# Optimization experiments

Measured on AMD Instinct MI355X. Metric: run time of the kernel, lower is better.

Reference implementation:

```python
import jax, jax.numpy as jnp
import numpy as np

N, D, E, L, H, F1, G, A = 4096, 256, 131072, 3, 4, 128, 16, 32

def setup_inputs() -> dict:
    key = jax.random.key(0)
    ks = jax.random.split(key, 12)
    s = lambda k, shape, fan: jax.random.normal(k, shape, jnp.float32) / np.sqrt(fan)
    return {
        "x": jax.random.normal(ks[0], (N, D), jnp.float32),
        "edge_attr": jax.random.uniform(ks[1], (E,), jnp.float32),
        "conv_Wself": s(ks[2], (L, D, D), D),
        "conv_Wnbr": s(ks[3], (L, D, D), D),
        "conv_b": jnp.zeros((L, D), jnp.float32),
        "bn_gamma": jnp.ones((L - 1, D), jnp.float32),
        "bn_beta": jnp.zeros((L - 1, D), jnp.float32),
        "bn_mean": jnp.zeros((L - 1, D), jnp.float32),
        "bn_var": jnp.ones((L - 1, D), jnp.float32),
        "Wqkv": s(ks[4], (3, D, D), D),
        "bqkv": jnp.zeros((3, D), jnp.float32),
        "Wo": s(ks[5], (D, D), D),
        "bo": jnp.zeros((D,), jnp.float32),
        "fc1_W": s(ks[6], (D, F1), D),
        "fc1_b": jnp.zeros((F1,), jnp.float32),
        "AW1": s(ks[7], (G, F1, A), F1),
        "Ab1": jnp.zeros((G, A), jnp.float32),
        "AW2": s(ks[8], (G, A, 1), A),
        "Ab2": jnp.zeros((G, 1), jnp.float32),
        "edge_index": jax.random.randint(ks[9], (2, E), 0, N, jnp.int32),
        "node_groups": jax.random.randint(ks[10], (N,), 0, G, jnp.int32),
    }


def reference(x, edge_attr, conv_Wself, conv_Wnbr, conv_b, bn_gamma, bn_beta,
              bn_mean, bn_var, Wqkv, bqkv, Wo, bo, fc1_W, fc1_b,
              AW1, Ab1, AW2, Ab2, edge_index, node_groups):
    src, dst = edge_index[0], edge_index[1]
    # message-passing conv stack (edge_attr only used by the last, non-attention layer)
    for i in range(L):
        msg = x[src]
        if i == L - 1:
            msg = msg * edge_attr[:, None]
        agg = jax.ops.segment_sum(msg, dst, num_segments=N)
        x = x @ conv_Wself[i] + agg @ conv_Wnbr[i] + conv_b[i]
        if i < L - 1:
            x = bn_gamma[i] * (x - bn_mean[i]) * jax.lax.rsqrt(bn_var[i] + 1e-5) + bn_beta[i]
            x = jax.nn.elu(x)
    # hierarchy self-attention over all N nodes (batch of 1), residual add
    dh = D // H
    q = (x @ Wqkv[0] + bqkv[0]).reshape(N, H, dh)
    k = (x @ Wqkv[1] + bqkv[1]).reshape(N, H, dh)
    v = (x @ Wqkv[2] + bqkv[2]).reshape(N, H, dh)
    scores = jnp.einsum('nhd,mhd->hnm', q, k) / np.sqrt(dh).astype(np.float32)
    attn = jax.nn.softmax(scores, axis=-1)
    o = jnp.einsum('hnm,mhd->nhd', attn, v).reshape(N, D) @ Wo + bo
    x = x + o
    feats = jax.nn.elu(x @ fc1_W + fc1_b)  # [N, F1]; dropout is eval no-op
    # MoE-style per-node group adapter routing: gather tiny MLP weights per node
    h = jax.nn.relu(jnp.einsum('nd,nda->na', feats, AW1[node_groups]) + Ab1[node_groups])
    out = jnp.einsum('na,nao->no', h, AW2[node_groups]) + Ab2[node_groups]  # [N, 1]
    return out
```

## Files before the change

kernel.cpp:

```cpp
#include <hip/hip_runtime.h>
#include <math.h>

#define NN   4096
#define DIM  256
#define NE   131072
#define NH   4
#define DH   64
#define F1D  128
#define NG   16
#define AD   32

typedef unsigned short u16;
typedef unsigned int   u32;
typedef _Float16 f16;
typedef __attribute__((ext_vector_type(8))) _Float16 half8;
typedef __attribute__((ext_vector_type(4))) float f32x4;

enum { EPI_BIAS = 0, EPI_BNELU = 1 };
enum { MEPI_WO = 0, MEPI_FC1 = 1 };

#define MFMA16(a, b, c) __builtin_amdgcn_mfma_f32_16x16x32_f16(a, b, c, 0, 0, 0)

__device__ inline u16 f2h(float x) { union { f16 f; u16 u; } c; c.f = (f16)x; return c.u; }
__device__ inline void split16(float x, u16& h, u16& l) {
    union { f16 f; u16 u; } ch, cl;
    ch.f = (f16)x;
    cl.f = (f16)(x - (float)ch.f);
    h = ch.u; l = cl.u;
}

__global__ void csr_count(const int* __restrict__ dst, int* __restrict__ cnt) {
    int e = blockIdx.x * 256 + threadIdx.x;
    atomicAdd(&cnt[dst[e]], 1);
}

__global__ __launch_bounds__(1024) void csr_scan(
    int* __restrict__ cnt, int* __restrict__ off)
{
    __shared__ int wsum[16];
    const int t = threadIdx.x;
    const int lane = t & 63;
    int4 v = *(const int4*)&cnt[t * 4];
    const int s = v.x + v.y + v.z + v.w;
    int acc = s;
    #pragma unroll
    for (int o = 1; o < 64; o <<= 1) {
        int u = __shfl_up(acc, o);
        if (lane >= o) acc += u;
    }
    if (lane == 63) wsum[t >> 6] = acc;
    __syncthreads();
    if (t < 16) {
        int w0 = wsum[t];
        int a2 = w0;
        #pragma unroll
        for (int o = 1; o < 16; o <<= 1) {
            int u = __shfl_up(a2, o);
            if (t >= o) a2 += u;
        }
        wsum[t] = a2 - w0;
    }
    __syncthreads();
    const int base = wsum[t >> 6] + (acc - s);
    off[t * 4 + 0] = base;
    off[t * 4 + 1] = base + v.x;
    off[t * 4 + 2] = base + v.x + v.y;
    off[t * 4 + 3] = base + v.x + v.y + v.z;
    *(int4*)&cnt[t * 4] = make_int4(0, 0, 0, 0);
    if (t == 1023) off[NN] = base + s;
}

__global__ void csr_fill(const int* __restrict__ dst, const int* __restrict__ src,
                         const float* __restrict__ eattr, const int* __restrict__ off,
                         int* __restrict__ cur, int* __restrict__ esrc,
                         float* __restrict__ ewt) {
    int e = blockIdx.x * 256 + threadIdx.x;
    int d = dst[e];
    int pos = off[d] + atomicAdd(&cur[d], 1);
    esrc[pos] = src[e];
    ewt[pos]  = eattr[e];
}

__global__ __launch_bounds__(256) void prep_kernel(
    const float* __restrict__ x,
    const float* __restrict__ Ws, const float* __restrict__ Wn,
    const float* __restrict__ Wqkv, const float* __restrict__ Wo,
    const float* __restrict__ fc1W,
    u16* __restrict__ xh, u16* __restrict__ xl,
    u16* __restrict__ wch, u16* __restrict__ wcl,
    u16* __restrict__ w4h, u16* __restrict__ w4l,
    u16* __restrict__ f1h, u16* __restrict__ f1l,
    int* __restrict__ cur)
{
    const int b = blockIdx.x;
    const int t = threadIdx.x;
    if (b < 1024) {
        const int gid = b * 256 + t;
        const float4 v = *(const float4*)&x[(size_t)gid * 4];
        u16 h[4], l[4];
        split16(v.x, h[0], l[0]); split16(v.y, h[1], l[1]);
        split16(v.z, h[2], l[2]); split16(v.w, h[3], l[3]);
        *(uint2*)&xh[(size_t)gid * 4] =
            make_uint2((u32)h[0] | ((u32)h[1] << 16), (u32)h[2] | ((u32)h[3] << 16));
        *(uint2*)&xl[(size_t)gid * 4] =
            make_uint2((u32)l[0] | ((u32)l[1] << 16), (u32)l[2] | ((u32)l[3] << 16));
    } else if (b < 1408) {
        const int gid = (b - 1024) * 256 + t;
        const int L = gid / 32768;
        const int rem = gid % 32768;
        const int m = rem / 128;
        const int k4 = (rem % 128) * 4;
        const float* S = Ws + (size_t)L * 65536;
        const float* Nb = Wn + (size_t)L * 65536;
        u16 h[4], l[4];
        #pragma unroll
        for (int j = 0; j < 4; ++j) {
            const int k = k4 + j;
            const float v = (k < 256) ? S[(size_t)k * 256 + m]
                                      : Nb[(size_t)(k - 256) * 256 + m];
            split16(v, h[j], l[j]);
        }
        const size_t o = (size_t)L * 131072 + (size_t)m * 512 + k4;
        *(uint2*)&wch[o] = make_uint2((u32)h[0] | ((u32)h[1] << 16), (u32)h[2] | ((u32)h[3] << 16));
        *(uint2*)&wcl[o] = make_uint2((u32)l[0] | ((u32)l[1] << 16), (u32)l[2] | ((u32)l[3] << 16));
    } else if (b < 1664) {
        const int gid = (b - 1408) * 256 + t;
        const int mat = gid / 16384;
        const int rem = gid % 16384;
        const int m = rem / 64;
        const int k4 = (rem % 64) * 4;
        const float* W = (mat < 3) ? Wqkv + (size_t)mat * 65536 : Wo;
        u16 h[4], l[4];
        #pragma unroll
        for (int j = 0; j < 4; ++j)
            split16(W[(size_t)(k4 + j) * 256 + m], h[j], l[j]);
        const size_t o = (size_t)mat * 65536 + (size_t)m * 256 + k4;
        *(uint2*)&w4h[o] = make_uint2((u32)h[0] | ((u32)h[1] << 16), (u32)h[2] | ((u32)h[3] << 16));
        *(uint2*)&w4l[o] = make_uint2((u32)l[0] | ((u32)l[1] << 16), (u32)l[2] | ((u32)l[3] << 16));
    } else if (b < 1696) {
        const int gid = (b - 1664) * 256 + t;
        const int m = gid / 64;
        const int k4 = (gid % 64) * 4;
        u16 h[4], l[4];
        #pragma unroll
        for (int j = 0; j < 4; ++j)
            split16(fc1W[(size_t)(k4 + j) * F1D + m], h[j], l[j]);
        const size_t o = (size_t)m * 256 + k4;
        *(uint2*)&f1h[o] = make_uint2((u32)h[0] | ((u32)h[1] << 16), (u32)h[2] | ((u32)h[3] << 16));
        *(uint2*)&f1l[o] = make_uint2((u32)l[0] | ((u32)l[1] << 16), (u32)l[2] | ((u32)l[3] << 16));
    } else {
        const int gid = (b - 1696) * 256 + t;
        if (gid < NN / 4) *(int4*)&cur[gid * 4] = make_int4(0, 0, 0, 0);
    }
}

template<bool LAST>
__global__ __launch_bounds__(256) void agg_kernel(
    const float* __restrict__ x, const int* __restrict__ esrc,
    const float* __restrict__ ewt, const int* __restrict__ off,
    u16* __restrict__ aggh, u16* __restrict__ aggl)
{
    const int node = blockIdx.x * 4 + (threadIdx.x >> 6);
    const int lane = threadIdx.x & 63;
    const int d4 = lane * 4;
    int j = off[node];
    const int j1 = off[node + 1];
    float4 acc = make_float4(0.f, 0.f, 0.f, 0.f);
    for (; j + 4 <= j1; j += 4) {
        const int s0 = esrc[j], s1 = esrc[j + 1], s2 = esrc[j + 2], s3 = esrc[j + 3];
        const float4 x0 = *(const float4*)&x[(size_t)s0 * DIM + d4];
        const float4 x1 = *(const float4*)&x[(size_t)s1 * DIM + d4];
        const float4 x2 = *(const float4*)&x[(size_t)s2 * DIM + d4];
        const float4 x3 = *(const float4*)&x[(size_t)s3 * DIM + d4];
        const float w0 = LAST ? ewt[j]     : 1.f;
        const float w1 = LAST ? ewt[j + 1] : 1.f;
        const float w2 = LAST ? ewt[j + 2] : 1.f;
        const float w3 = LAST ? ewt[j + 3] : 1.f;
        acc.x = fmaf(x0.x, w0, acc.x); acc.y = fmaf(x0.y, w0, acc.y);
        acc.z = fmaf(x0.z, w0, acc.z); acc.w = fmaf(x0.w, w0, acc.w);
        acc.x = fmaf(x1.x, w1, acc.x); acc.y = fmaf(x1.y, w1, acc.y);
        acc.z = fmaf(x1.z, w1, acc.z); acc.w = fmaf(x1.w, w1, acc.w);
        acc.x = fmaf(x2.x, w2, acc.x); acc.y = fmaf(x2.y, w2, acc.y);
        acc.z = fmaf(x2.z, w2, acc.z); acc.w = fmaf(x2.w, w2, acc.w);
        acc.x = fmaf(x3.x, w3, acc.x); acc.y = fmaf(x3.y, w3, acc.y);
        acc.z = fmaf(x3.z, w3, acc.z); acc.w = fmaf(x3.w, w3, acc.w);
    }
    for (; j < j1; ++j) {
        const int s = esrc[j];
        const float w = LAST ? ewt[j] : 1.f;
        const float4 xv = *(const float4*)&x[(size_t)s * DIM + d4];
        acc.x = fmaf(xv.x, w, acc.x); acc.y = fmaf(xv.y, w, acc.y);
        acc.z = fmaf(xv.z, w, acc.z); acc.w = fmaf(xv.w, w, acc.w);
    }
    u16 h[4], l[4];
    split16(acc.x, h[0], l[0]); split16(acc.y, h[1], l[1]);
    split16(acc.z, h[2], l[2]); split16(acc.w, h[3], l[3]);
    *(uint2*)&aggh[(size_t)node * DIM + d4] =
        make_uint2((u32)h[0] | ((u32)h[1] << 16), (u32)h[2] | ((u32)h[3] << 16));
    *(uint2*)&aggl[(size_t)node * DIM + d4] =
        make_uint2((u32)l[0] | ((u32)l[1] << 16), (u32)l[2] | ((u32)l[3] << 16));
}

template<int EPI>
__global__ __launch_bounds__(256) void conv_mfma(
    const u16* __restrict__ xh, const u16* __restrict__ xl,
    const u16* __restrict__ gh, const u16* __restrict__ gl,
    const u16* __restrict__ bth, const u16* __restrict__ btl,
    const float* __restrict__ bias,
    const float* __restrict__ gamma, const float* __restrict__ beta,
    const float* __restrict__ bnmean, const float* __restrict__ bnvar,
    float* __restrict__ outf, u16* __restrict__ oh, u16* __restrict__ ol)
{
    __shared__ u16 lds[13824];
    u16* As_h = lds;
    u16* As_l = lds + 2304;
    u16* Bs_h = lds + 4608;
    u16* Bs_l = lds + 9216;
    #define TKP 72

    const int tid  = threadIdx.x;
    const int row0 = blockIdx.y * 32;
    const int col0 = blockIdx.x * 64;

    const int w   = tid >> 6;
    const int l15 = tid & 15, h4 = (tid & 63) >> 4;
    const int rh  = w & 1, ch = w >> 1;
    const int arow = tid >> 3, acs = (tid & 7) * 8;
    const int brow = tid & 63, bseg = tid >> 6;
    const int bc = bseg * 16;

    uint4 sah, sal, sbh0, sbh1, sbl0, sbl1;
    {
        sah = *((const uint4*)&xh[(size_t)(row0 + arow) * DIM + acs]);
        sal = *((const uint4*)&xl[(size_t)(row0 + arow) * DIM + acs]);
        const u16* pbh = bth + (size_t)(col0 + brow) * 512 + bc;
        const u16* pbl = btl + (size_t)(col0 + brow) * 512 + bc;
        sbh0 = ((const uint4*)pbh)[0]; sbh1 = ((const uint4*)pbh)[1];
        sbl0 = ((const uint4*)pbl)[0]; sbl1 = ((const uint4*)pbl)[1];
    }

    const f32x4 z4 = {0.f, 0.f, 0.f, 0.f};
    f32x4 acc[2] = {z4, z4};

    for (int kt = 0; kt < 8; ++kt) {
        *(uint4*)&As_h[arow * TKP + acs] = sah;
        *(uint4*)&As_l[arow * TKP + acs] = sal;
        *(uint4*)&Bs_h[brow * TKP + bc]     = sbh0;
        *(uint4*)&Bs_h[brow * TKP + bc + 8] = sbh1;
        *(uint4*)&Bs_l[brow * TKP + bc]     = sbl0;
        *(uint4*)&Bs_l[brow * TKP + bc + 8] = sbl1;
        if (kt + 1 < 8) {
            const int kn = kt + 1;
            const u16 *pah, *pal;
            if (kn < 4) {
                pah = xh + (size_t)(row0 + arow) * DIM + kn * 64 + acs;
                pal = xl + (size_t)(row0 + arow) * DIM + kn * 64 + acs;
            } else {
                pah = gh + (size_t)(row0 + arow) * DIM + (kn - 4) * 64 + acs;
                pal = gl + (size_t)(row0 + arow) * DIM + (kn - 4) * 64 + acs;
            }
            sah = *((const uint4*)pah);
            sal = *((const uint4*)pal);
            const u16* pbh = bth + (size_t)(col0 + brow) * 512 + kn * 64 + bc;
            const u16* pbl = btl + (size_t)(col0 + brow) * 512 + kn * 64 + bc;
            sbh0 = ((const uint4*)pbh)[0]; sbh1 = ((const uint4*)pbh)[1];
            sbl0 = ((const uint4*)pbl)[0]; sbl1 = ((const uint4*)pbl)[1];
        }
        __syncthreads();

        __builtin_amdgcn_s_setprio(1);
        #pragma unroll
        for (int kc = 0; kc < 2; ++kc) {
            const int dc = kc * 32 + h4 * 8;
            half8 afh, afl, bfh[2], bfl[2];
            afh = *(const half8*)&As_h[(rh * 16 + l15) * TKP + dc];
            afl = *(const half8*)&As_l[(rh * 16 + l15) * TKP + dc];
            #pragma unroll
            for (int bb = 0; bb < 2; ++bb) {
                const int r = ch * 32 + bb * 16 + l15;
                bfh[bb] = *(const half8*)&Bs_h[r * TKP + dc];
                bfl[bb] = *(const half8*)&Bs_l[r * TKP + dc];
            }
            #pragma unroll
            for (int bb = 0; bb < 2; ++bb) {
                acc[bb] = MFMA16(afh, bfh[bb], acc[bb]);
                acc[bb] = MFMA16(afh, bfl[bb], acc[bb]);
                acc[bb] = MFMA16(afl, bfh[bb], acc[bb]);
            }
        }
        __builtin_amdgcn_s_setprio(0);
        __syncthreads();
    }

    #pragma unroll
    for (int bb = 0; bb < 2; ++bb) {
        const int c  = col0 + ch * 32 + bb * 16 + l15;
        const int r0 = row0 + rh * 16 + h4 * 4;
        #pragma unroll
        for (int i = 0; i < 4; ++i) {
            const int r = r0 + i;
            float t = acc[bb][i] + bias[c];
            if (EPI == EPI_BNELU) {
                t = gamma[c] * (t - bnmean[c]) * rsqrtf(bnvar[c] + 1e-5f) + beta[c];
                t = t > 0.f ? t : expm1f(t);
            }
            outf[(size_t)r * DIM + c] = t;
            u16 hh, ll;
            split16(t, hh, ll);
            oh[(size_t)r * DIM + c] = hh;
            ol[(size_t)r * DIM + c] = ll;
        }
    }
    #undef TKP
}

__global__ __launch_bounds__(256) void qkv_mfma(
    const u16* __restrict__ xh, const u16* __restrict__ xl,
    const u16* __restrict__ wth, const u16* __restrict__ wtl,
    const float* __restrict__ bias,
    u16* __restrict__ qh_o, u16* __restrict__ ql_o,
    u16* __restrict__ kh_o, u16* __restrict__ kl_o,
    u16* __restrict__ vt_o)
{
    __shared__ u16 lds[4 * 4608];
    u16* As_h = lds;
    u16* As_l = lds + 4608;
    u16* Bs_h = lds + 9216;
    u16* Bs_l = lds + 13824;
    #define TKP 72

    const int tid  = threadIdx.x;
    const int row0 = blockIdx.y * 64;
    const int mat  = blockIdx.x >> 2;
    const int col0 = (blockIdx.x & 3) * 64;
    const float* biasp = bias + mat * DIM;

    const int w   = tid >> 6;
    const int l15 = tid & 15, h4 = (tid & 63) >> 4;
    const int rh  = w & 1, ch = w >> 1;
    const int lrow = tid & 63, lseg = tid >> 6;
    const int lc = lseg * 16;

    const size_t brow = (size_t)(mat * 256 + col0 + lrow) * 256;
    uint4 sah0, sah1, sal0, sal1, sbh0, sbh1, sbl0, sbl1;
    {
        const u16* pah = xh + (size_t)(row0 + lrow) * DIM + lc;
        const u16* pal = xl + (size_t)(row0 + lrow) * DIM + lc;
        sah0 = ((const uint4*)pah)[0]; sah1 = ((const uint4*)pah)[1];
        sal0 = ((const uint4*)pal)[0]; sal1 = ((const uint4*)pal)[1];
        sbh0 = ((const uint4*)(wth + brow + lc))[0]; sbh1 = ((const uint4*)(wth + brow + lc))[1];
        sbl0 = ((const uint4*)(wtl + brow + lc))[0]; sbl1 = ((const uint4*)(wtl + brow + lc))[1];
    }

    const f32x4 z4 = {0.f, 0.f, 0.f, 0.f};
    f32x4 acc[2][2] = {{z4, z4}, {z4, z4}};

    for (int kt = 0; kt < 4; ++kt) {
        *(uint4*)&As_h[lrow * TKP + lc]     = sah0;
        *(uint4*)&As_h[lrow * TKP + lc + 8] = sah1;
        *(uint4*)&As_l[lrow * TKP + lc]     = sal0;
        *(uint4*)&As_l[lrow * TKP + lc + 8] = sal1;
        *(uint4*)&Bs_h[lrow * TKP + lc]     = sbh0;
        *(uint4*)&Bs_h[lrow * TKP + lc + 8] = sbh1;
        *(uint4*)&Bs_l[lrow * TKP + lc]     = sbl0;
        *(uint4*)&Bs_l[lrow * TKP + lc + 8] = sbl1;
        if (kt + 1 < 4) {
            const int kb = (kt + 1) * 64 + lc;
            const u16* pah = xh + (size_t)(row0 + lrow) * DIM + kb;
            const u16* pal = xl + (size_t)(row0 + lrow) * DIM + kb;
            sah0 = ((const uint4*)pah)[0]; sah1 = ((const uint4*)pah)[1];
            sal0 = ((const uint4*)pal)[0]; sal1 = ((const uint4*)pal)[1];
            sbh0 = ((const uint4*)(wth + brow + kb))[0]; sbh1 = ((const uint4*)(wth + brow + kb))[1];
            sbl0 = ((const uint4*)(wtl + brow + kb))[0]; sbl1 = ((const uint4*)(wtl + brow + kb))[1];
        }
        __syncthreads();

        __builtin_amdgcn_s_setprio(1);
        #pragma unroll
        for (int kc = 0; kc < 2; ++kc) {
            const int dc = kc * 32 + h4 * 8;
            half8 afh[2], afl[2], bfh[2], bfl[2];
            #pragma unroll
            for (int ab = 0; ab < 2; ++ab) {
                const int r = rh * 32 + ab * 16 + l15;
                afh[ab] = *(const half8*)&As_h[r * TKP + dc];
                afl[ab] = *(const half8*)&As_l[r * TKP + dc];
            }
            #pragma unroll
            for (int bb = 0; bb < 2; ++bb) {
                const int r = ch * 32 + bb * 16 + l15;
                bfh[bb] = *(const half8*)&Bs_h[r * TKP + dc];
                bfl[bb] = *(const half8*)&Bs_l[r * TKP + dc];
            }
            #pragma unroll
            for (int ab = 0; ab < 2; ++ab)
                #pragma unroll
                for (int bb = 0; bb < 2; ++bb) {
                    acc[ab][bb] = MFMA16(afh[ab], bfh[bb], acc[ab][bb]);
                    acc[ab][bb] = MFMA16(afh[ab], bfl[bb], acc[ab][bb]);
                    acc[ab][bb] = MFMA16(afl[ab], bfh[bb], acc[ab][bb]);
                }
        }
        __builtin_amdgcn_s_setprio(0);
        __syncthreads();
    }

    const float s = (mat == 0) ? 0.125f : 1.0f;
    u16* oph = (mat == 0) ? qh_o : kh_o;
    u16* opl = (mat == 0) ? ql_o : kl_o;
    #pragma unroll
    for (int ab = 0; ab < 2; ++ab)
        #pragma unroll
        for (int bb = 0; bb < 2; ++bb) {
            const int c  = col0 + ch * 32 + bb * 16 + l15;
            const int r0 = row0 + rh * 32 + ab * 16 + h4 * 4;
            if (mat < 2) {
                #pragma unroll
                for (int i = 0; i < 4; ++i) {
                    const int r = r0 + i;
                    const float t = (acc[ab][bb][i] + biasp[c]) * s;
                    u16 hh, ll;
                    split16(t, hh, ll);
                    oph[(size_t)r * DIM + c] = hh;
                    opl[(size_t)r * DIM + c] = ll;
                }
            } else {
                u16 v[4];
                #pragma unroll
                for (int i = 0; i < 4; ++i)
                    v[i] = f2h(acc[ab][bb][i] + biasp[c]);
                *(uint2*)&vt_o[(size_t)c * NN + r0] =
                    make_uint2((u32)v[0] | ((u32)v[1] << 16), (u32)v[2] | ((u32)v[3] << 16));
            }
        }
    #undef TKP
}

template<int MEPI>
__global__ __launch_bounds__(256) void mfma_gemm32(
    const u16* __restrict__ Ah, const u16* __restrict__ Al,
    const u16* __restrict__ Bth, const u16* __restrict__ Btl,
    const float* __restrict__ bias, const float* __restrict__ resid,
    float* __restrict__ outf, u16* __restrict__ outh, u16* __restrict__ outl,
    int K, int M)
{
    __shared__ u16 lds[13824];
    u16* As_h = lds;
    u16* As_l = lds + 2304;
    u16* Bs_h = lds + 4608;
    u16* Bs_l = lds + 9216;
    #define TKP 72

    const int tid  = threadIdx.x;
    const int row0 = blockIdx.y * 32;
    const int col0 = blockIdx.x * 64;

    const int w   = tid >> 6;
    const int l15 = tid & 15, h4 = (tid & 63) >> 4;
    const int rh  = w & 1, ch = w >> 1;
    const int arow = tid >> 3, acs = (tid & 7) * 8;
    const int brow = tid & 63, bseg = tid >> 6;
    const int bc = bseg * 16;

    uint4 sah, sal, sbh0, sbh1, sbl0, sbl1;
    {
        sah = *((const uint4*)&Ah[(size_t)(row0 + arow) * K + acs]);
        sal = *((const uint4*)&Al[(size_t)(row0 + arow) * K + acs]);
        const u16* pbh = Bth + (size_t)(col0 + brow) * K + bc;
        const u16* pbl = Btl + (size_t)(col0 + brow) * K + bc;
        sbh0 = ((const uint4*)pbh)[0]; sbh1 = ((const uint4*)pbh)[1];
        sbl0 = ((const uint4*)pbl)[0]; sbl1 = ((const uint4*)pbl)[1];
    }

    const f32x4 z4 = {0.f, 0.f, 0.f, 0.f};
    f32x4 acc[2] = {z4, z4};
    const int NKT2 = K / 64;

    for (int kt = 0; kt < NKT2; ++kt) {
        *(uint4*)&As_h[arow * TKP + acs] = sah;
        *(uint4*)&As_l[arow * TKP + acs] = sal;
        *(uint4*)&Bs_h[brow * TKP + bc]     = sbh0;
        *(uint4*)&Bs_h[brow * TKP + bc + 8] = sbh1;
        *(uint4*)&Bs_l[brow * TKP + bc]     = sbl0;
        *(uint4*)&Bs_l[brow * TKP + bc + 8] = sbl1;
        if (kt + 1 < NKT2) {
            const int kb = (kt + 1) * 64;
            sah = *((const uint4*)&Ah[(size_t)(row0 + arow) * K + kb + acs]);
            sal = *((const uint4*)&Al[(size_t)(row0 + arow) * K + kb + acs]);
            const u16* pbh = Bth + (size_t)(col0 + brow) * K + kb + bc;
            const u16* pbl = Btl + (size_t)(col0 + brow) * K + kb + bc;
            sbh0 = ((const uint4*)pbh)[0]; sbh1 = ((const uint4*)pbh)[1];
            sbl0 = ((const uint4*)pbl)[0]; sbl1 = ((const uint4*)pbl)[1];
        }
        __syncthreads();

        __builtin_amdgcn_s_setprio(1);
        #pragma unroll
        for (int kc = 0; kc < 2; ++kc) {
            const int dc = kc * 32 + h4 * 8;
            half8 afh, afl, bfh[2], bfl[2];
            afh = *(const half8*)&As_h[(rh * 16 + l15) * TKP + dc];
            afl = *(const half8*)&As_l[(rh * 16 + l15) * TKP + dc];
            #pragma unroll
            for (int bb = 0; bb < 2; ++bb) {
                const int r = ch * 32 + bb * 16 + l15;
                bfh[bb] = *(const half8*)&Bs_h[r * TKP + dc];
                bfl[bb] = *(const half8*)&Bs_l[r * TKP + dc];
            }
            #pragma unroll
            for (int bb = 0; bb < 2; ++bb) {
                acc[bb] = MFMA16(afh, bfh[bb], acc[bb]);
                acc[bb] = MFMA16(afh, bfl[bb], acc[bb]);
                acc[bb] = MFMA16(afl, bfh[bb], acc[bb]);
            }
        }
        __builtin_amdgcn_s_setprio(0);
        __syncthreads();
    }

    #pragma unroll
    for (int bb = 0; bb < 2; ++bb) {
        const int c  = col0 + ch * 32 + bb * 16 + l15;
        const int r0 = row0 + rh * 16 + h4 * 4;
        #pragma unroll
        for (int i = 0; i < 4; ++i) {
            const int r = r0 + i;
            float t = acc[bb][i] + bias[c];
            if (MEPI == MEPI_WO) {
                t += resid[(size_t)r * M + c];
                u16 hh, ll;
                split16(t, hh, ll);
                outh[(size_t)r * M + c] = hh;
                outl[(size_t)r * M + c] = ll;
            } else {
                t = t > 0.f ? t : expm1f(t);
                outf[(size_t)r * M + c] = t;
            }
        }
    }
    #undef TKP
}

#define QB 128
#define KB 64
#define NSPLIT 4
#define NKT (NN / KB)
#define KP 72

__global__ __launch_bounds__(512, 2) void attn_kernel(
    const u16* __restrict__ qhi, const u16* __restrict__ qlo,
    const u16* __restrict__ khi, const u16* __restrict__ klo,
    const u16* __restrict__ vT,
    float* __restrict__ op0, float* __restrict__ op1,
    float* __restrict__ op2, float* __restrict__ op3,
    float* __restrict__ mpart, float* __restrict__ lpart)
{
    __shared__ u16 lds[37120];
    u16* Kh0 = lds;
    u16* Kl0 = lds + 4608;
    u16* Vt0 = lds + 9216;
    u16* Kh1 = lds + 13824;
    u16* Kl1 = lds + 18432;
    u16* Vt1 = lds + 23040;
    u16* Pb  = lds + 27648;
    u16* Qh  = lds;
    u16* Ql  = lds + 13824;
    float* frow = (float*)(lds + 36864);

    const int tid = threadIdx.x;
    const int h   = blockIdx.y;
    const int q0  = blockIdx.x * QB;
    const int sp  = blockIdx.z;
    const int kt0 = sp * (NKT / NSPLIT);
    const int kt1 = kt0 + NKT / NSPLIT;

    const int w   = tid >> 6;
    const int l15 = tid & 15, h4 = (tid & 63) >> 4;
    const int lrow = tid & 63, lseg = tid >> 6;
    const int gq8 = h * DH + lseg * 8;

    {
        const int qrow = tid >> 2, qseg = tid & 3;
        const u16* s0 = qhi + (size_t)(q0 + qrow) * DIM + h * DH + qseg * 16;
        const u16* s1 = qlo + (size_t)(q0 + qrow) * DIM + h * DH + qseg * 16;
        uint4 a = ((const uint4*)s0)[0], b = ((const uint4*)s0)[1];
        uint4 c = ((const uint4*)s1)[0], d = ((const uint4*)s1)[1];
        *(uint4*)&Qh[qrow * KP + qseg * 16]     = a;
        *(uint4*)&Qh[qrow * KP + qseg * 16 + 8] = b;
        *(uint4*)&Ql[qrow * KP + qseg * 16]     = c;
        *(uint4*)&Ql[qrow * KP + qseg * 16 + 8] = d;
    }

    uint4 rk, rl, rv;
    auto load_tile = [&](int kt_ld) {
        const int key0 = kt_ld * KB;
        rk = *(const uint4*)(khi + (size_t)(key0 + lrow) * DIM + gq8);
        rl = *(const uint4*)(klo + (size_t)(key0 + lrow) * DIM + gq8);
        rv = *(const uint4*)(vT + (size_t)(h * DH + lrow) * NN + key0 + lseg * 8);
    };
    load_tile(kt0);
    __syncthreads();

    half8 qf[2][2];
    #pragma unroll
    for (int kc = 0; kc < 2; ++kc) {
        const int r = w * 16 + l15;
        const int dc = kc * 32 + h4 * 8;
        qf[kc][0] = *(const half8*)&Qh[r * KP + dc];
        qf[kc][1] = *(const half8*)&Ql[r * KP + dc];
    }
    __syncthreads();

    auto stage_to = [&](u16* Kh, u16* Kl, u16* Vt) {
        *(uint4*)&Kh[lrow * KP + lseg * 8] = rk;
        *(uint4*)&Kl[lrow * KP + lseg * 8] = rl;
        *(uint4*)&Vt[lrow * KP + lseg * 8] = rv;
    };

    stage_to(Kh0, Kl0, Vt0);
    load_tile(kt0 + 1);
    __syncthreads();

    const f32x4 z4 = {0.f, 0.f, 0.f, 0.f};
    f32x4 oacc[4] = {z4, z4, z4, z4};
    float m_run[4], l_run[4];
    #pragma unroll
    for (int i = 0; i < 4; ++i) { m_run[i] = -3.0e38f; l_run[i] = 0.f; }

    auto tile_body = [&](int t, u16* Kc, u16* Lc, u16* Vc,
                         u16* Kn, u16* Ln, u16* Vn) {
        if (t + 1 < kt1) stage_to(Kn, Ln, Vn);
        if (t + 2 < kt1) load_tile(t + 2);

        f32x4 sc[4] = {z4, z4, z4, z4};
        __builtin_amdgcn_s_setprio(1);
        #pragma unroll
        for (int kc = 0; kc < 2; ++kc) {
            const int dc = kc * 32 + h4 * 8;
            half8 kfh[4], kfl[4];
            #pragma unroll
            for (int kcb = 0; kcb < 4; ++kcb) {
                const int r = kcb * 16 + l15;
                kfh[kcb] = *(const half8*)&Kc[r * KP + dc];
                kfl[kcb] = *(const half8*)&Lc[r * KP + dc];
            }
            #pragma unroll
            for (int kcb = 0; kcb < 4; ++kcb) {
                sc[kcb] = MFMA16(qf[kc][0], kfh[kcb], sc[kcb]);
                sc[kcb] = MFMA16(qf[kc][0], kfl[kcb], sc[kcb]);
                sc[kcb] = MFMA16(qf[kc][1], kfh[kcb], sc[kcb]);
            }
        }
        __builtin_amdgcn_s_setprio(0);

        float pm[4];
        #pragma unroll
        for (int i = 0; i < 4; ++i) {
            float v = fmaxf(fmaxf(sc[0][i], sc[1][i]), fmaxf(sc[2][i], sc[3][i]));
            #pragma unroll
            for (int off = 1; off < 16; off <<= 1)
                v = fmaxf(v, __shfl_xor(v, off));
            pm[i] = v;
        }
        const int ok = (pm[0] - m_run[0] <= 8.f) && (pm[1] - m_run[1] <= 8.f) &&
                       (pm[2] - m_run[2] <= 8.f) && (pm[3] - m_run[3] <= 8.f);
        float p[4][4];
        if (__all(ok)) {
            #pragma unroll
            for (int i = 0; i < 4; ++i) {
                p[0][i] = __expf(sc[0][i] - m_run[i]);
                p[1][i] = __expf(sc[1][i] - m_run[i]);
                p[2][i] = __expf(sc[2][i] - m_run[i]);
                p[3][i] = __expf(sc[3][i] - m_run[i]);
                float ls = (p[0][i] + p[1][i]) + (p[2][i] + p[3][i]);
                #pragma unroll
                for (int off = 1; off < 16; off <<= 1) ls += __shfl_xor(ls, off);
                l_run[i] += ls;
            }
        } else {
            float fr[4];
            #pragma unroll
            for (int i = 0; i < 4; ++i) {
                const float mnew = fmaxf(m_run[i], pm[i]);
                fr[i] = __expf(m_run[i] - mnew);
                m_run[i] = mnew;
                p[0][i] = __expf(sc[0][i] - mnew);
                p[1][i] = __expf(sc[1][i] - mnew);
                p[2][i] = __expf(sc[2][i] - mnew);
                p[3][i] = __expf(sc[3][i] - mnew);
                float ls = (p[0][i] + p[1][i]) + (p[2][i] + p[3][i]);
                #pragma unroll
                for (int off = 1; off < 16; off <<= 1) ls += __shfl_xor(ls, off);
                l_run[i] = l_run[i] * fr[i] + ls;
            }
            if (l15 == 0) {
                #pragma unroll
                for (int i = 0; i < 4; ++i)
                    frow[w * 16 + h4 * 4 + i] = fr[i];
            }
            const float frq = frow[w * 16 + l15];
            #pragma unroll
            for (int db = 0; db < 4; ++db) oacc[db] *= frq;
        }
        #pragma unroll
        for (int kcb = 0; kcb < 4; ++kcb) {
            const int kk = kcb * 16 + l15;
            #pragma unroll
            for (int i = 0; i < 4; ++i)
                Pb[(w * 16 + h4 * 4 + i) * KP + kk] = f2h(p[kcb][i]);
        }
        __builtin_amdgcn_s_setprio(1);
        #pragma unroll
        for (int kc = 0; kc < 2; ++kc) {
            const half8 pf = *(const half8*)&Pb[(w * 16 + l15) * KP + kc * 32 + h4 * 8];
            #pragma unroll
            for (int db = 0; db < 4; ++db) {
                const half8 vf = *(const half8*)&Vc[(db * 16 + l15) * KP + kc * 32 + h4 * 8];
                oacc[db] = MFMA16(vf, pf, oacc[db]);
            }
        }
        __builtin_amdgcn_s_setprio(0);
        __syncthreads();
    };

    for (int t = kt0; t < kt1; t += 2) {
        tile_body(t,     Kh0, Kl0, Vt0, Kh1, Kl1, Vt1);
        tile_body(t + 1, Kh1, Kl1, Vt1, Kh0, Kl0, Vt0);
    }

    float* ob = (sp == 0) ? op0 : ((sp == 1) ? op1 : ((sp == 2) ? op2 : op3));
    #pragma unroll
    for (int db = 0; db < 4; ++db)
        *(f32x4*)&ob[(size_t)(q0 + w * 16 + l15) * DIM + h * DH + db * 16 + h4 * 4] = oacc[db];
    if (l15 == 0) {
        #pragma unroll
        for (int i = 0; i < 4; ++i) {
            const int r = w * 16 + h4 * 4 + i;
            mpart[((size_t)sp * NN + q0 + r) * NH + h] = m_run[i];
            lpart[((size_t)sp * NN + q0 + r) * NH + h] = l_run[i];
        }
    }
}

__global__ __launch_bounds__(256) void attn_combine(
    const float* __restrict__ o0, const float* __restrict__ o1,
    const float* __restrict__ o2, const float* __restrict__ o3,
    const float* __restrict__ mp, const float* __restrict__ lp,
    u16* __restrict__ ohi, u16* __restrict__ olo)
{
    const int gid = blockIdx.x * 256 + threadIdx.x;
    const int row = gid >> 6;
    const int c4  = (gid & 63) * 4;
    const int h   = c4 >> 6;
    float m[4], wgt[4];
    #pragma unroll
    for (int z = 0; z < 4; ++z) m[z] = mp[((size_t)z * NN + row) * NH + h];
    const float M = fmaxf(fmaxf(m[0], m[1]), fmaxf(m[2], m[3]));
    float den = 0.f;
    #pragma unroll
    for (int z = 0; z < 4; ++z) {
        wgt[z] = __expf(m[z] - M);
        den += lp[((size_t)z * NN + row) * NH + h] * wgt[z];
    }
    const float inv = 1.f / den;
    const float4 a = *(const float4*)&o0[(size_t)row * DIM + c4];
    const float4 b = *(const float4*)&o1[(size_t)row * DIM + c4];
    const float4 c = *(const float4*)&o2[(size_t)row * DIM + c4];
    const float4 d = *(const float4*)&o3[(size_t)row * DIM + c4];
    float r[4];
    r[0] = (a.x * wgt[0] + b.x * wgt[1] + c.x * wgt[2] + d.x * wgt[3]) * inv;
    r[1] = (a.y * wgt[0] + b.y * wgt[1] + c.y * wgt[2] + d.y * wgt[3]) * inv;
    r[2] = (a.z * wgt[0] + b.z * wgt[1] + c.z * wgt[2] + d.z * wgt[3]) * inv;
    r[3] = (a.w * wgt[0] + b.w * wgt[1] + c.w * wgt[2] + d.w * wgt[3]) * inv;
    u16 hh[4], ll[4];
    #pragma unroll
    for (int j = 0; j < 4; ++j) split16(r[j], hh[j], ll[j]);
    *(uint2*)&ohi[(size_t)row * DIM + c4] =
        make_uint2((u32)hh[0] | ((u32)hh[1] << 16), (u32)hh[2] | ((u32)hh[3] << 16));
    *(uint2*)&olo[(size_t)row * DIM + c4] =
        make_uint2((u32)ll[0] | ((u32)ll[1] << 16), (u32)ll[2] | ((u32)ll[3] << 16));
}

__global__ __launch_bounds__(256) void adapter_kernel(
    const float* __restrict__ feats, const int* __restrict__ grp,
    const float* __restrict__ AW1, const float* __restrict__ Ab1,
    const float* __restrict__ AW2, const float* __restrict__ Ab2,
    float* __restrict__ out)
{
    const int wv = threadIdx.x >> 6;
    const int n = blockIdx.x * 4 + wv;
    const int lane = threadIdx.x & 63;
    __shared__ float f[4][F1D];
    f[wv][lane]      = feats[(size_t)n * F1D + lane];
    f[wv][lane + 64] = feats[(size_t)n * F1D + 64 + lane];
    const int g = grp[n];
    const float* W1 = AW1 + (size_t)g * F1D * AD;
    const int a = lane & 31;
    const int half = lane >> 5;
    float hsum = 0.f;
    for (int d = 0; d < 64; ++d)
        hsum = fmaf(f[wv][half * 64 + d], W1[(half * 64 + d) * AD + a], hsum);
    hsum += __shfl_xor(hsum, 32);
    hsum = fmaxf(hsum + Ab1[g * AD + a], 0.f);
    float p = hsum * AW2[g * AD + a];
    #pragma unroll
    for (int mm = 1; mm < 32; mm <<= 1) p += __shfl_xor(p, mm);
    if (lane == 0) out[n] = p + Ab2[g];
}

extern "C" void kernel_launch(void* const* d_in, const int* in_sizes, int n_in,
                              void* d_out, int out_size, void* d_ws, size_t ws_size,
                              hipStream_t stream)
{
    const float* x_in   = (const float*)d_in[0];
    const float* eattr  = (const float*)d_in[1];
    const float* Wself  = (const float*)d_in[2];
    const float* Wnbr   = (const float*)d_in[3];
    const float* convb  = (const float*)d_in[4];
    const float* gamma  = (const float*)d_in[5];
    const float* beta   = (const float*)d_in[6];
    const float* bnmean = (const float*)d_in[7];
    const float* bnvar  = (const float*)d_in[8];
    const float* Wqkv   = (const float*)d_in[9];
    const float* bqkv   = (const float*)d_in[10];
    const float* Wo     = (const float*)d_in[11];
    const float* bo     = (const float*)d_in[12];
    const float* fc1W   = (const float*)d_in[13];
    const float* fc1b   = (const float*)d_in[14];
    const float* AW1    = (const float*)d_in[15];
    const float* Ab1    = (const float*)d_in[16];
    const float* AW2    = (const float*)d_in[17];
    const float* Ab2    = (const float*)d_in[18];
    const int*   eidx   = (const int*)d_in[19];
    const int*   grp    = (const int*)d_in[20];
    const int* srcArr = eidx;
    const int* dstArr = eidx + NE;

    float* fws = (float*)d_ws;
    const size_t NM = (size_t)NN * DIM;
    float* bufA  = fws;
    float* bufB  = fws + NM;
    float* bufC  = fws + 2 * NM;
    float* feats = fws + 3 * NM;
    float* mpart = fws + 3 * NM + NM / 2;
    float* lpart = mpart + 4 * NN * NH;
    u16* up = (u16*)(lpart + 4 * NN * NH);
    u16* xpAh = up;             u16* xpAl = xpAh + NM;
    u16* xpBh = xpAl + NM;      u16* xpBl = xpBh + NM;
    u16* aggh = xpBl + NM;      u16* aggl = aggh + NM;
    u16* qh = aggl + NM;        u16* ql = qh + NM;
    u16* kh = ql + NM;          u16* kl = kh + NM;
    u16* vt = kl + NM;
    u16* wcath = vt + NM;
    u16* wcatl = wcath + 3 * 131072;
    u16* wt4h  = wcatl + 3 * 131072;
    u16* wt4l  = wt4h + 4 * 65536;
    u16* fc1h  = wt4l + 4 * 65536;
    u16* fc1l  = fc1h + 32768;
    int*   esrc = (int*)(fc1l + 32768);
    float* ewt  = (float*)(esrc + NE);
    int* off    = (int*)(ewt + NE);
    int* cur    = off + NN + 1;
    float* outp = (float*)d_out;

    float* op2 = (float*)xpAh;
    float* op3 = (float*)xpBh;

    prep_kernel<<<1700, 256, 0, stream>>>(
        x_in, Wself, Wnbr, Wqkv, Wo, fc1W,
        xpAh, xpAl, wcath, wcatl, wt4h, wt4l, fc1h, fc1l, cur);

    csr_count<<<NE / 256, 256, 0, stream>>>(dstArr, cur);
    csr_scan<<<1, 1024, 0, stream>>>(cur, off);
    csr_fill<<<NE / 256, 256, 0, stream>>>(dstArr, srcArr, eattr, off, cur, esrc, ewt);

    const dim3 gc(DIM / 64, NN / 32);
    const int rgrid = NN * DIM / 4 / 256;

    agg_kernel<false><<<NN / 4, 256, 0, stream>>>(x_in, esrc, ewt, off, aggh, aggl);
    conv_mfma<EPI_BNELU><<<gc, 256, 0, stream>>>(
        xpAh, xpAl, aggh, aggl, wcath, wcatl, convb,
        gamma, beta, bnmean, bnvar, bufA, xpBh, xpBl);
    agg_kernel<false><<<NN / 4, 256, 0, stream>>>(bufA, esrc, ewt, off, aggh, aggl);
    conv_mfma<EPI_BNELU><<<gc, 256, 0, stream>>>(
        xpBh, xpBl, aggh, aggl, wcath + 131072, wcatl + 131072, convb + DIM,
        gamma + DIM, beta + DIM, bnmean + DIM, bnvar + DIM, bufC, xpAh, xpAl);
    agg_kernel<true><<<NN / 4, 256, 0, stream>>>(bufC, esrc, ewt, off, aggh, aggl);
    conv_mfma<EPI_BIAS><<<gc, 256, 0, stream>>>(
        xpAh, xpAl, aggh, aggl, wcath + 262144, wcatl + 262144, convb + 2 * DIM,
        nullptr, nullptr, nullptr, nullptr, bufA, xpBh, xpBl);

    qkv_mfma<<<dim3(12, NN / 64), 256, 0, stream>>>(
        xpBh, xpBl, wt4h, wt4l, bqkv, qh, ql, kh, kl, vt);

    attn_kernel<<<dim3(NN / QB, NH, NSPLIT), 512, 0, stream>>>(
        qh, ql, kh, kl, vt, bufB, bufC, op2, op3, mpart, lpart);
    attn_combine<<<rgrid, 256, 0, stream>>>(
        bufB, bufC, op2, op3, mpart, lpart, qh, ql);

    mfma_gemm32<MEPI_WO><<<dim3(DIM / 64, NN / 32), 256, 0, stream>>>(
        qh, ql, wt4h + 3 * 65536, wt4l + 3 * 65536, bo, bufA,
        nullptr, kh, kl, DIM, DIM);

    mfma_gemm32<MEPI_FC1><<<dim3(F1D / 64, NN / 32), 256, 0, stream>>>(
        kh, kl, fc1h, fc1l, fc1b, nullptr, feats, nullptr, nullptr, DIM, F1D);

    adapter_kernel<<<NN / 4, 256, 0, stream>>>(feats, grp, AW1, Ab1, AW2, Ab2, outp);
}
```

Baseline: 233.7 us.

## Transpose QK^T MFMA so P stays in registers, replace LDS P buffer with shuffles

The QK^T MFMA operands are swapped so each lane holds scores for a single query row (column of the tile). The row max and sum now need only two cross-lane shuffles, and each lane keeps one scalar m/l, so the LDS round-trip for the rescale factor goes away. The P tile is packed to fp16 and redistributed into the PV MFMA operand layout with ds_bpermute shuffles instead of being written to and read back from an LDS buffer. This shrinks LDS use, which may allow more blocks per CU, but adds shuffle instructions.

```diff
diff --git a/kernel.cpp b/kernel.cpp
--- a/kernel.cpp
+++ b/kernel.cpp
@@ -555,17 +555,15 @@
     float* __restrict__ op2, float* __restrict__ op3,
     float* __restrict__ mpart, float* __restrict__ lpart)
 {
-    __shared__ u16 lds[37120];
+    __shared__ u16 lds[27648];
     u16* Kh0 = lds;
     u16* Kl0 = lds + 4608;
     u16* Vt0 = lds + 9216;
     u16* Kh1 = lds + 13824;
     u16* Kl1 = lds + 18432;
     u16* Vt1 = lds + 23040;
-    u16* Pb  = lds + 27648;
     u16* Qh  = lds;
     u16* Ql  = lds + 13824;
-    float* frow = (float*)(lds + 36864);
 
     const int tid = threadIdx.x;
     const int h   = blockIdx.y;
@@ -623,9 +621,9 @@
 
     const f32x4 z4 = {0.f, 0.f, 0.f, 0.f};
     f32x4 oacc[4] = {z4, z4, z4, z4};
-    float m_run[4], l_run[4];
-    #pragma unroll
-    for (int i = 0; i < 4; ++i) { m_run[i] = -3.0e38f; l_run[i] = 0.f; }
+    float m_run = -3.0e38f, l_run = 0.f;
+    const int sl0 = (h4 & 1) * 32 + l15;
+    const int sl1 = sl0 + 16;
 
     auto tile_body = [&](int t, u16* Kc, u16* Lc, u16* Vc,
                          u16* Kn, u16* Ln, u16* Vn) {
@@ -646,77 +644,82 @@
             }
             #pragma unroll
             for (int kcb = 0; kcb < 4; ++kcb) {
-                sc[kcb] = MFMA16(qf[kc][0], kfh[kcb], sc[kcb]);
-                sc[kcb] = MFMA16(qf[kc][0], kfl[kcb], sc[kcb]);
-                sc[kcb] = MFMA16(qf[kc][1], kfh[kcb], sc[kcb]);
+                sc[kcb] = MFMA16(kfh[kcb], qf[kc][0], sc[kcb]);
+                sc[kcb] = MFMA16(kfl[kcb], qf[kc][0], sc[kcb]);
+                sc[kcb] = MFMA16(kfh[kcb], qf[kc][1], sc[kcb]);
             }
         }
         __builtin_amdgcn_s_setprio(0);
 
-        float pm[4];
-        #pragma unroll
-        for (int i = 0; i < 4; ++i) {
-            float v = fmaxf(fmaxf(sc[0][i], sc[1][i]), fmaxf(sc[2][i], sc[3][i]));
-            #pragma unroll
-            for (int off = 1; off < 16; off <<= 1)
-                v = fmaxf(v, __shfl_xor(v, off));
-            pm[i] = v;
-        }
-        const int ok = (pm[0] - m_run[0] <= 8.f) && (pm[1] - m_run[1] <= 8.f) &&
-                       (pm[2] - m_run[2] <= 8.f) && (pm[3] - m_run[3] <= 8.f);
+        float c0 = fmaxf(fmaxf(sc[0][0], sc[0][1]), fmaxf(sc[0][2], sc[0][3]));
+        float c1 = fmaxf(fmaxf(sc[1][0], sc[1][1]), fmaxf(sc[1][2], sc[1][3]));
+        float c2 = fmaxf(fmaxf(sc[2][0], sc[2][1]), fmaxf(sc[2][2], sc[2][3]));
+        float c3 = fmaxf(fmaxf(sc[3][0], sc[3][1]), fmaxf(sc[3][2], sc[3][3]));
+        float pm = fmaxf(fmaxf(c0, c1), fmaxf(c2, c3));
+        pm = fmaxf(pm, __shfl_xor(pm, 16));
+        pm = fmaxf(pm, __shfl_xor(pm, 32));
+
         float p[4][4];
-        if (__all(ok)) {
-            #pragma unroll
-            for (int i = 0; i < 4; ++i) {
-                p[0][i] = __expf(sc[0][i] - m_run[i]);
-                p[1][i] = __expf(sc[1][i] - m_run[i]);
-                p[2][i] = __expf(sc[2][i] - m_run[i]);
-                p[3][i] = __expf(sc[3][i] - m_run[i]);
-                float ls = (p[0][i] + p[1][i]) + (p[2][i] + p[3][i]);
-                #pragma unroll
-                for (int off = 1; off < 16; off <<= 1) ls += __shfl_xor(ls, off);
-                l_run[i] += ls;
-            }
+        float base, fr = 1.f;
+        int resc;
+        if (__all(pm - m_run <= 8.f)) {
+            base = m_run;
+            resc = 0;
         } else {
-            float fr[4];
-            #pragma unroll
-            for (int i = 0; i < 4; ++i) {
-                const float mnew = fmaxf(m_run[i], pm[i]);
-                fr[i] = __expf(m_run[i] - mnew);
-                m_run[i] = mnew;
-                p[0][i] = __expf(sc[0][i] - mnew);
-                p[1][i] = __expf(sc[1][i] - mnew);
-                p[2][i] = __expf(sc[2][i] - mnew);
-                p[3][i] = __expf(sc[3][i] - mnew);
-                float ls = (p[0][i] + p[1][i]) + (p[2][i] + p[3][i]);
-                #pragma unroll
-                for (int off = 1; off < 16; off <<= 1) ls += __shfl_xor(ls, off);
-                l_run[i] = l_run[i] * fr[i] + ls;
-            }
-            if (l15 == 0) {
-                #pragma unroll
-                for (int i = 0; i < 4; ++i)
-                    frow[w * 16 + h4 * 4 + i] = fr[i];
-            }
-            const float frq = frow[w * 16 + l15];
-            #pragma unroll
-            for (int db = 0; db < 4; ++db) oacc[db] *= frq;
-        }
+            const float mnew = fmaxf(m_run, pm);
+            fr = __expf(m_run - mnew);
+            m_run = mnew;
+            base = mnew;
+            resc = 1;
+        }
+        #pragma unroll
+        for (int kcb = 0; kcb < 4; ++kcb)
+            #pragma unroll
+            for (int i = 0; i < 4; ++i)
+                p[kcb][i] = __expf(sc[kcb][i] - base);
+        float s0s = (p[0][0] + p[0][1]) + (p[0][2] + p[0][3]);
+        float s1s = (p[1][0] + p[1][1]) + (p[1][2] + p[1][3]);
+        float s2s = (p[2][0] + p[2][1]) + (p[2][2] + p[2][3]);
+        float s3s = (p[3][0] + p[3][1]) + (p[3][2] + p[3][3]);
+        float ls = (s0s + s1s) + (s2s + s3s);
+        ls += __shfl_xor(ls, 16);
+        ls += __shfl_xor(ls, 32);
+        if (resc) {
+            l_run = l_run * fr + ls;
+            #pragma unroll
+            for (int db = 0; db < 4; ++db) oacc[db] *= fr;
+        } else {
+            l_run += ls;
+        }
+
+        u32 pk01[4], pk23[4];
         #pragma unroll
         for (int kcb = 0; kcb < 4; ++kcb) {
-            const int kk = kcb * 16 + l15;
-            #pragma unroll
-            for (int i = 0; i < 4; ++i)
-                Pb[(w * 16 + h4 * 4 + i) * KP + kk] = f2h(p[kcb][i]);
-        }
+            pk01[kcb] = (u32)f2h(p[kcb][0]) | ((u32)f2h(p[kcb][1]) << 16);
+            pk23[kcb] = (u32)f2h(p[kcb][2]) | ((u32)f2h(p[kcb][3]) << 16);
+        }
+
+        const int hiSel = h4 >> 1;
         __builtin_amdgcn_s_setprio(1);
         #pragma unroll
         for (int kc = 0; kc < 2; ++kc) {
-            const half8 pf = *(const half8*)&Pb[(w * 16 + l15) * KP + kc * 32 + h4 * 8];
+            const u32 a0 = (u32)__shfl((int)pk01[kc * 2], sl0);
+            const u32 a1 = (u32)__shfl((int)pk23[kc * 2], sl0);
+            const u32 a2 = (u32)__shfl((int)pk01[kc * 2], sl1);
+            const u32 a3 = (u32)__shfl((int)pk23[kc * 2], sl1);
+            const u32 b0 = (u32)__shfl((int)pk01[kc * 2 + 1], sl0);
+            const u32 b1 = (u32)__shfl((int)pk23[kc * 2 + 1], sl0);
+            const u32 b2 = (u32)__shfl((int)pk01[kc * 2 + 1], sl1);
+            const u32 b3 = (u32)__shfl((int)pk23[kc * 2 + 1], sl1);
+            union { half8 v; u32 u[4]; } pf;
+            pf.u[0] = hiSel ? b0 : a0;
+            pf.u[1] = hiSel ? b1 : a1;
+            pf.u[2] = hiSel ? b2 : a2;
+            pf.u[3] = hiSel ? b3 : a3;
             #pragma unroll
             for (int db = 0; db < 4; ++db) {
                 const half8 vf = *(const half8*)&Vc[(db * 16 + l15) * KP + kc * 32 + h4 * 8];
-                oacc[db] = MFMA16(vf, pf, oacc[db]);
+                oacc[db] = MFMA16(vf, pf.v, oacc[db]);
             }
         }
         __builtin_amdgcn_s_setprio(0);
@@ -732,13 +735,10 @@
     #pragma unroll
     for (int db = 0; db < 4; ++db)
         *(f32x4*)&ob[(size_t)(q0 + w * 16 + l15) * DIM + h * DH + db * 16 + h4 * 4] = oacc[db];
-    if (l15 == 0) {
-        #pragma unroll
-        for (int i = 0; i < 4; ++i) {
-            const int r = w * 16 + h4 * 4 + i;
-            mpart[((size_t)sp * NN + q0 + r) * NH + h] = m_run[i];
-            lpart[((size_t)sp * NN + q0 + r) * NH + h] = l_run[i];
-        }
+    if (h4 == 0) {
+        const int r = w * 16 + l15;
+        mpart[((size_t)sp * NN + q0 + r) * NH + h] = m_run;
+        lpart[((size_t)sp * NN + q0 + r) * NH + h] = l_run;
     }
 }
 
```

New measurement: 211.6 us. 1.1x faster.
